# Optimization experiments

Measured on AMD Instinct MI355X. Metric: run time of the kernel, lower is better.

## Reference

```python
import jax, jax.numpy as jnp
import numpy as np

N_IN = 256      # n_in
N_OUT = 1024    # n_out
D_IN = 256      # power-of-2 adjusted input dim (padding = 0 here)
D_OUT = 1024    # stack * D_IN
STACK = 4
BATCH = 65536


def build_H(D):
    # Sylvester (unnormalized) Hadamard matrix, as in build_H of the repo.
    H = np.array([[1.0]], dtype=np.float32)
    while H.shape[0] < D:
        H = np.block([[H, H], [H, -H]])
    return jnp.asarray(H)


def setup_inputs() -> dict:
    key = jax.random.key(0)
    k0, k1, k2 = jax.random.split(key, 3)
    x = jax.random.normal(k0, (BATCH, N_IN), dtype=jnp.float32)
    s1 = jnp.ones((STACK, D_IN), dtype=jnp.float32) * 0.01
    s2 = jnp.ones((STACK, D_IN), dtype=jnp.float32) * 0.01
    g_mu = jnp.zeros((STACK, D_IN), dtype=jnp.float32)
    g_rho = jax.random.uniform(k1, (STACK, D_IN), dtype=jnp.float32,
                               minval=-5.0, maxval=-4.0)
    epsilon = jax.random.normal(k2, (STACK, D_IN), dtype=jnp.float32)
    return {"x": x, "s1": s1, "s2": s2, "g_mu": g_mu,
            "g_rho": g_rho, "epsilon": epsilon}


def reference(x, s1, s2, g_mu, g_rho, epsilon):
    H = build_H(D_IN)  # (D, D)

    # One square WHVI sample: W = diag(s1) @ H @ diag(g) @ (H * s2)
    # (FWHT.apply(M) == H @ M for the Sylvester Hadamard; s2 scales columns.)
    def square_term(s1k, s2k, gk):
        HS2 = H * s2k[None, :]                       # H @ diag(s2)
        return s1k[:, None] * (H @ (gk[:, None] * HS2))  # (D, D)

    g_sigma = jax.nn.softplus(g_rho)
    mu_term = jax.vmap(square_term)(s1, s2, g_mu)              # (stack, D, D)
    sigma_term = jax.vmap(square_term)(s1, s2, g_sigma * epsilon)
    W = (mu_term + sigma_term).reshape(D_OUT, D_IN)            # torch.cat over stack

    # Pad input features up to D_IN (no-op here since padding == 0).
    x_padded = jnp.pad(x, ((0, 0), (0, D_IN - N_IN)))
    out = x_padded @ W.T                                       # F.linear
    return out[..., :N_OUT]
```

## Files before the change

### kernel.cpp

```cpp
#include <hip/hip_runtime.h>

#define D_IN 256
#define D_OUT 1024
#define STACK 4
#define BATCH 65536

__device__ __forceinline__ void fwht256(float v[4], int lane) {
    float a0 = v[0] + v[1];
    float a1 = v[0] - v[1];
    float a2 = v[2] + v[3];
    float a3 = v[2] - v[3];
    v[0] = a0 + a2;
    v[2] = a0 - a2;
    v[1] = a1 + a3;
    v[3] = a1 - a3;
#pragma unroll
    for (int d = 1; d < 64; d <<= 1) {
        const bool upper = (lane & d) != 0;
#pragma unroll
        for (int j = 0; j < 4; ++j) {
            float o = __shfl_xor(v[j], d, 64);
            v[j] = upper ? (o - v[j]) : (v[j] + o);
        }
    }
}

__global__ __launch_bounds__(256) void whvi_fwht_kernel(
    const float* __restrict__ x,
    const float* __restrict__ s1,
    const float* __restrict__ s2,
    const float* __restrict__ g_mu,
    const float* __restrict__ g_rho,
    const float* __restrict__ eps,
    float* __restrict__ out,
    int nrows)
{
    const int lane = threadIdx.x & 63;
    const int waveInBlock = threadIdx.x >> 6;
    const int wavesPerBlock = blockDim.x >> 6;
    const int gwave = blockIdx.x * wavesPerBlock + waveInBlock;
    const int nwaves = gridDim.x * wavesPerBlock;

    const int e0 = lane << 2;

    float s1v[STACK][4], s2v[STACK][4], gv[STACK][4];
#pragma unroll
    for (int k = 0; k < STACK; ++k) {
        const float4 a = *reinterpret_cast<const float4*>(s1   + k * D_IN + e0);
        const float4 b = *reinterpret_cast<const float4*>(s2   + k * D_IN + e0);
        const float4 m = *reinterpret_cast<const float4*>(g_mu + k * D_IN + e0);
        const float4 r = *reinterpret_cast<const float4*>(g_rho + k * D_IN + e0);
        const float4 e = *reinterpret_cast<const float4*>(eps  + k * D_IN + e0);
        s1v[k][0] = a.x; s1v[k][1] = a.y; s1v[k][2] = a.z; s1v[k][3] = a.w;
        s2v[k][0] = b.x; s2v[k][1] = b.y; s2v[k][2] = b.z; s2v[k][3] = b.w;
        gv[k][0] = m.x + log1pf(expf(r.x)) * e.x;
        gv[k][1] = m.y + log1pf(expf(r.y)) * e.y;
        gv[k][2] = m.z + log1pf(expf(r.z)) * e.z;
        gv[k][3] = m.w + log1pf(expf(r.w)) * e.w;
    }

    for (int row = gwave; row < nrows; row += nwaves) {
        const float4 xi = *reinterpret_cast<const float4*>(x + (size_t)row * D_IN + e0);
        float xr[4] = {xi.x, xi.y, xi.z, xi.w};

#pragma unroll
        for (int k = 0; k < STACK; ++k) {
            float v[4];
#pragma unroll
            for (int j = 0; j < 4; ++j) v[j] = xr[j] * s2v[k][j];
            fwht256(v, lane);
#pragma unroll
            for (int j = 0; j < 4; ++j) v[j] *= gv[k][j];
            fwht256(v, lane);
            float4 o;
            o.x = v[0] * s1v[k][0];
            o.y = v[1] * s1v[k][1];
            o.z = v[2] * s1v[k][2];
            o.w = v[3] * s1v[k][3];
            *reinterpret_cast<float4*>(out + (size_t)row * D_OUT + k * D_IN + e0) = o;
        }
    }
}

extern "C" void kernel_launch(void* const* d_in, const int* in_sizes, int n_in,
                              void* d_out, int out_size, void* d_ws, size_t ws_size,
                              hipStream_t stream) {
    const float* x     = (const float*)d_in[0];
    const float* s1    = (const float*)d_in[1];
    const float* s2    = (const float*)d_in[2];
    const float* g_mu  = (const float*)d_in[3];
    const float* g_rho = (const float*)d_in[4];
    const float* eps   = (const float*)d_in[5];
    float* out = (float*)d_out;

    const int nrows = in_sizes[0] / D_IN;
    const int block = 256;
    const int grid  = 2048;
    whvi_fwht_kernel<<<grid, block, 0, stream>>>(x, s1, s2, g_mu, g_rho, eps,
                                                 out, nrows);
}
```

Before: 390.6 us.

## Materialize WHVI weight in bf16 and compute output with MFMA GEMM

Instead of applying two 256-point FWHTs per row per stack with wave shuffles, a small pre-kernel builds the dense 1024x256 weight matrix, converts it to bf16 and stores it pre-swizzled in MFMA fragment layout. A second kernel converts x to bf16 in registers and runs 16x16x32 bf16 MFMA tiles over all 64 output column tiles. This trades shuffle-heavy ALU work for matrix-core throughput, at the cost of bf16 rounding of both inputs and weights, which may break accuracy tolerance. Output stores are strided scalar writes rather than vectorized.

```diff
diff --git a/kernel.cpp b/kernel.cpp
--- a/kernel.cpp
+++ b/kernel.cpp
@@ -1,19 +1,21 @@
 #include <hip/hip_runtime.h>
+#include <hip/hip_bf16.h>
 
-#define D_IN 256
-#define D_OUT 1024
-#define STACK 4
-#define BATCH 65536
+#define D 256
+#define DOUT 1024
+#define STACKS 4
+#define NTILES 64
+
+typedef __attribute__((ext_vector_type(8))) short bf16x8;
+typedef __attribute__((ext_vector_type(4))) float f32x4;
 
 __device__ __forceinline__ void fwht256(float v[4], int lane) {
     float a0 = v[0] + v[1];
     float a1 = v[0] - v[1];
     float a2 = v[2] + v[3];
     float a3 = v[2] - v[3];
-    v[0] = a0 + a2;
-    v[2] = a0 - a2;
-    v[1] = a1 + a3;
-    v[3] = a1 - a3;
+    v[0] = a0 + a2; v[2] = a0 - a2;
+    v[1] = a1 + a3; v[3] = a1 - a3;
 #pragma unroll
     for (int d = 1; d < 64; d <<= 1) {
         const bool upper = (lane & d) != 0;
@@ -25,59 +27,92 @@
     }
 }
 
-__global__ __launch_bounds__(256) void whvi_fwht_kernel(
-    const float* __restrict__ x,
-    const float* __restrict__ s1,
-    const float* __restrict__ s2,
-    const float* __restrict__ g_mu,
-    const float* __restrict__ g_rho,
-    const float* __restrict__ eps,
-    float* __restrict__ out,
-    int nrows)
+__global__ __launch_bounds__(256) void build_bpack(
+    const float* __restrict__ s1, const float* __restrict__ s2,
+    const float* __restrict__ g_mu, const float* __restrict__ g_rho,
+    const float* __restrict__ eps, __hip_bfloat16* __restrict__ bpack)
+{
+    const int wid  = blockIdx.x * 4 + (threadIdx.x >> 6);
+    const int lane = threadIdx.x & 63;
+    const int k = wid & 255;
+    const int s = wid >> 8;
+
+    const int e0 = lane * 4;
+    float v[4];
+#pragma unroll
+    for (int j = 0; j < 4; ++j) {
+        const int e = e0 + j;
+        const float g = g_mu[s * D + e]
+                      + log1pf(expf(g_rho[s * D + e])) * eps[s * D + e];
+        v[j] = (__builtin_popcount(e & k) & 1) ? -g : g;
+    }
+    fwht256(v, lane);
+    const float s2k = s2[s * D + k];
+#pragma unroll
+    for (int j = 0; j < 4; ++j) {
+        const int e = e0 + j;
+        const int o = s * D + e;
+        const float w = s1[s * D + e] * v[j] * s2k;
+        const int addr = ((o >> 4) * 8 + (k >> 5)) * 512
+                       + (((k >> 3) & 3) * 16 + (o & 15)) * 8 + (k & 7);
+        bpack[addr] = __float2bfloat16(w);
+    }
+}
+
+__device__ __forceinline__ unsigned pk2(float a, float b) {
+    union { __hip_bfloat162 h; unsigned u; } c;
+    c.h = __float22bfloat162_rn(float2{a, b});
+    return c.u;
+}
+__device__ __forceinline__ bf16x8 as_frag(const unsigned u[4]) {
+    union { unsigned u[4]; bf16x8 v; } c;
+    c.u[0] = u[0]; c.u[1] = u[1]; c.u[2] = u[2]; c.u[3] = u[3];
+    return c.v;
+}
+
+__global__ __launch_bounds__(256) void whvi_gemm(
+    const float* __restrict__ x, const bf16x8* __restrict__ bpack,
+    float* __restrict__ out, int nrows)
 {
     const int lane = threadIdx.x & 63;
-    const int waveInBlock = threadIdx.x >> 6;
-    const int wavesPerBlock = blockDim.x >> 6;
-    const int gwave = blockIdx.x * wavesPerBlock + waveInBlock;
-    const int nwaves = gridDim.x * wavesPerBlock;
+    const int wid  = threadIdx.x >> 6;
+    const int rbase = (blockIdx.x * 4 + wid) * 32;
+    if (rbase >= nrows) return;
+    const int rlo = lane & 15;
+    const int g4  = lane >> 4;
 
-    const int e0 = lane << 2;
-
-    float s1v[STACK][4], s2v[STACK][4], gv[STACK][4];
+    unsigned a_pk[2][8][4];
 #pragma unroll
-    for (int k = 0; k < STACK; ++k) {
-        const float4 a = *reinterpret_cast<const float4*>(s1   + k * D_IN + e0);
-        const float4 b = *reinterpret_cast<const float4*>(s2   + k * D_IN + e0);
-        const float4 m = *reinterpret_cast<const float4*>(g_mu + k * D_IN + e0);
-        const float4 r = *reinterpret_cast<const float4*>(g_rho + k * D_IN + e0);
-        const float4 e = *reinterpret_cast<const float4*>(eps  + k * D_IN + e0);
-        s1v[k][0] = a.x; s1v[k][1] = a.y; s1v[k][2] = a.z; s1v[k][3] = a.w;
-        s2v[k][0] = b.x; s2v[k][1] = b.y; s2v[k][2] = b.z; s2v[k][3] = b.w;
-        gv[k][0] = m.x + log1pf(expf(r.x)) * e.x;
-        gv[k][1] = m.y + log1pf(expf(r.y)) * e.y;
-        gv[k][2] = m.z + log1pf(expf(r.z)) * e.z;
-        gv[k][3] = m.w + log1pf(expf(r.w)) * e.w;
+    for (int rf = 0; rf < 2; ++rf) {
+        const float* xr = x + (size_t)(rbase + rf * 16 + rlo) * D + g4 * 8;
+#pragma unroll
+        for (int kb = 0; kb < 8; ++kb) {
+            const float4 f0 = *reinterpret_cast<const float4*>(xr + kb * 32);
+            const float4 f1 = *reinterpret_cast<const float4*>(xr + kb * 32 + 4);
+            a_pk[rf][kb][0] = pk2(f0.x, f0.y);
+            a_pk[rf][kb][1] = pk2(f0.z, f0.w);
+            a_pk[rf][kb][2] = pk2(f1.x, f1.y);
+            a_pk[rf][kb][3] = pk2(f1.z, f1.w);
+        }
     }
 
-    for (int row = gwave; row < nrows; row += nwaves) {
-        const float4 xi = *reinterpret_cast<const float4*>(x + (size_t)row * D_IN + e0);
-        float xr[4] = {xi.x, xi.y, xi.z, xi.w};
-
+    const bf16x8* bp = bpack + lane;
+    for (int nt = 0; nt < NTILES; ++nt) {
+        f32x4 acc0 = {0.f, 0.f, 0.f, 0.f};
+        f32x4 acc1 = {0.f, 0.f, 0.f, 0.f};
 #pragma unroll
-        for (int k = 0; k < STACK; ++k) {
-            float v[4];
+        for (int kb = 0; kb < 8; ++kb) {
+            const bf16x8 b = bp[(nt * 8 + kb) * 64];
+            acc0 = __builtin_amdgcn_mfma_f32_16x16x32_bf16(
+                       as_frag(a_pk[0][kb]), b, acc0, 0, 0, 0);
+            acc1 = __builtin_amdgcn_mfma_f32_16x16x32_bf16(
+                       as_frag(a_pk[1][kb]), b, acc1, 0, 0, 0);
+        }
+        float* o = out + (size_t)rbase * DOUT + nt * 16 + rlo;
 #pragma unroll
-            for (int j = 0; j < 4; ++j) v[j] = xr[j] * s2v[k][j];
-            fwht256(v, lane);
-#pragma unroll
-            for (int j = 0; j < 4; ++j) v[j] *= gv[k][j];
-            fwht256(v, lane);
-            float4 o;
-            o.x = v[0] * s1v[k][0];
-            o.y = v[1] * s1v[k][1];
-            o.z = v[2] * s1v[k][2];
-            o.w = v[3] * s1v[k][3];
-            *reinterpret_cast<float4*>(out + (size_t)row * D_OUT + k * D_IN + e0) = o;
+        for (int q = 0; q < 4; ++q) {
+            o[(size_t)(g4 * 4 + q) * DOUT]      = acc0[q];
+            o[(size_t)(16 + g4 * 4 + q) * DOUT] = acc1[q];
         }
     }
 }
@@ -93,9 +128,11 @@
     const float* eps   = (const float*)d_in[5];
     float* out = (float*)d_out;
 
-    const int nrows = in_sizes[0] / D_IN;
-    const int block = 256;
-    const int grid  = 2048;
-    whvi_fwht_kernel<<<grid, block, 0, stream>>>(x, s1, s2, g_mu, g_rho, eps,
-                                                 out, nrows);
+    __hip_bfloat16* bpack = (__hip_bfloat16*)d_ws;
+
+    build_bpack<<<256, 256, 0, stream>>>(s1, s2, g_mu, g_rho, eps, bpack);
+
+    const int nrows = in_sizes[0] / D;
+    const int grid  = nrows / 128;
+    whvi_gemm<<<grid, 256, 0, stream>>>(x, (const bf16x8*)bpack, out, nrows);
 }
```

New measurement: 405.7 us. 1.04x slower.
